# Kernel tuning notes

Hardware: AMD Instinct MI355X
Metric: run time of the kernel (lower is better)

The kernel has to match this reference:

```python
import jax, jax.numpy as jnp
import numpy as np

LOG2 = float(np.log(2.0))

def ssp(x):
    # shifted softplus: softplus(x) - log(2)
    return jax.nn.softplus(x) - LOG2

def setup_inputs() -> dict:
    key = jax.random.key(0)
    ks = jax.random.split(key, 16)
    N, E, F = 50000, 800000, 128  # atoms, interactions, feature/filter dim
    s = 0.05
    return {
        "x": jax.random.normal(ks[0], (N, F), jnp.float32),
        "dijk": jax.random.uniform(ks[1], (E, F), jnp.float32),
        "idx_j": jax.random.randint(ks[2], (E,), 0, N),
        "seg_i": jnp.sort(jax.random.randint(ks[3], (E,), 0, N)),
        "seg_j": jnp.arange(E),
        "seg_i_sum": N,
        "W1": jax.random.normal(ks[4], (F, F), jnp.float32) * s,
        "b1": jnp.zeros((F,), jnp.float32),
        "W2": jax.random.normal(ks[5], (F, F), jnp.float32) * s,
        "b2": jnp.zeros((F,), jnp.float32),
        "W_in2fac": jax.random.normal(ks[6], (F, F), jnp.float32) * s,
        "W_fac2out": jax.random.normal(ks[7], (F, F), jnp.float32) * s,
        "b_fac2out": jnp.zeros((F,), jnp.float32),
        "W_dense": jax.random.normal(ks[8], (F, F), jnp.float32) * s,
        "b_dense": jnp.zeros((F,), jnp.float32),
    }

def reference(x, dijk, idx_j, seg_i, seg_j, seg_i_sum,
              W1, b1, W2, b2, W_in2fac, W_fac2out, b_fac2out, W_dense, b_dense):
    E = dijk.shape[0]
    # --- CFnetFilter: dense -> dense -> segment-sum over seg_j ---
    h = ssp(dijk @ W1 + b1)                        # [E, F]
    w_ijk = ssp(h @ W2 + b2)                       # [E, F]
    w_ij = jax.ops.segment_sum(w_ijk, seg_j, num_segments=E)  # [E, F]
    # --- CFConv: in2fac -> gather idx_j -> filter mult -> segment-sum seg_i -> fac2out ---
    f = x @ W_in2fac                               # [N, F]
    f = f[idx_j]                                   # gather, [E, F]
    wf = w_ij * f                                  # [E, F]
    conv = jax.ops.segment_sum(wf, seg_i, num_segments=seg_i_sum)  # [N, F]
    c = ssp(conv @ W_fac2out + b_fac2out)          # [N, F]
    # --- residual dense ---
    v = c @ W_dense + b_dense                      # [N, F]
    y = x + v
    return (y, v)
```

## Files before the change

kernel.cpp:

```cpp
#include <hip/hip_runtime.h>

#define F 128

typedef __attribute__((ext_vector_type(8))) short bf16x8;
typedef __attribute__((ext_vector_type(4))) float f32x4;


__device__ __forceinline__ short f2bf(float f) {
  union { float f; unsigned u; } v; v.f = f;
  unsigned r = (v.u + 0x7FFFu + ((v.u >> 16) & 1u)) >> 16;
  return (short)r;
}

__device__ __forceinline__ unsigned cvt_pk_bf16(float a, float b) {
  unsigned d;
  asm("v_cvt_pk_bf16_f32 %0, %1, %2" : "=v"(d) : "v"(a), "v"(b));
  return d;
}

__device__ __forceinline__ float sspf(float x) {
  float t = __expf(-fabsf(x));
  return fmaxf(x, 0.0f) + __logf(1.0f + t) - 0.69314718055994530942f;
}

__device__ __forceinline__ int h_idx(int row, int k) {
  int chunk = k >> 3;
  int sw = chunk ^ (row & 15);
  return row * 128 + sw * 8 + (k & 7);
}

__device__ __forceinline__ int wfb_idx(int row, int c) {
  return row * 128 + (c ^ ((row & 4) << 2));
}

__device__ __forceinline__ bf16x8 load_bfrag_g(const unsigned short* __restrict__ W,
                                               int nt, int kb, int lane) {
  return *(const bf16x8*)(W + (((nt * 4 + kb) * 64 + lane) << 3));
}

__device__ __forceinline__ bf16x8 load_afrag_f32(const float* __restrict__ p, bool valid) {
  union { bf16x8 v; unsigned u[4]; } r;
  if (valid) {
    const float4* q = (const float4*)p;
    float4 x0 = q[0], x1 = q[1];
    r.u[0] = cvt_pk_bf16(x0.x, x0.y);
    r.u[1] = cvt_pk_bf16(x0.z, x0.w);
    r.u[2] = cvt_pk_bf16(x1.x, x1.y);
    r.u[3] = cvt_pk_bf16(x1.z, x1.w);
  } else {
    r.u[0] = r.u[1] = r.u[2] = r.u[3] = 0u;
  }
  return r.v;
}

__global__ void prep_weights(const float* __restrict__ W1, const float* __restrict__ W2,
                             const float* __restrict__ Wi2f, const float* __restrict__ Wf2o,
                             const float* __restrict__ Wd, unsigned short* __restrict__ out) {
  int t = blockIdx.x * 256 + threadIdx.x;
  int m = t >> 14;
  int idx = t & 16383;
  int k = idx >> 7, n = idx & 127;
  const float* W = (m == 0) ? W1 : (m == 1) ? W2 : (m == 2) ? Wi2f : (m == 3) ? Wf2o : Wd;
  float v = W[idx];
  int nt = n >> 4, kb = k >> 5;
  int lane = (((k >> 3) & 3) << 4) | (n & 15);
  int j = k & 7;
  int dst = (((nt * 4 + kb) * 64 + lane) << 3) | j;
  out[(m << 14) + dst] = (unsigned short)f2bf(v);
}

__global__ __launch_bounds__(256, 4) void f_kernel(const float* __restrict__ x,
                                                   const unsigned short* __restrict__ wfrag,
                                                   float* __restrict__ f, int N) {
  const int tid = threadIdx.x;
  const int lane = tid & 63, wv = tid >> 6;
  const int quad = lane >> 4, ln = lane & 15;
  const int r0 = blockIdx.x * 128;
  const unsigned short* Wf = wfrag + 2 * 16384;

  bf16x8 a1[2][4];
#pragma unroll
  for (int mt = 0; mt < 2; ++mt) {
    int row = r0 + wv * 32 + mt * 16 + ln;
    bool valid = row < N;
    const float* rp = x + (size_t)row * F + quad * 8;
#pragma unroll
    for (int kb = 0; kb < 4; ++kb) a1[mt][kb] = load_afrag_f32(rp + kb * 32, valid);
  }

#pragma unroll
  for (int nt = 0; nt < 8; ++nt) {
    f32x4 acc0 = {0, 0, 0, 0}, acc1 = {0, 0, 0, 0};
#pragma unroll
    for (int kb = 0; kb < 4; ++kb) {
      bf16x8 b = load_bfrag_g(Wf, nt, kb, lane);
      acc0 = __builtin_amdgcn_mfma_f32_16x16x32_bf16(a1[0][kb], b, acc0, 0, 0, 0);
      acc1 = __builtin_amdgcn_mfma_f32_16x16x32_bf16(a1[1][kb], b, acc1, 0, 0, 0);
    }
    int col = nt * 16 + ln;
#pragma unroll
    for (int mt = 0; mt < 2; ++mt) {
#pragma unroll
      for (int r = 0; r < 4; ++r) {
        int row = r0 + wv * 32 + mt * 16 + quad * 4 + r;
        if (row < N) f[(size_t)row * F + col] = (mt == 0) ? acc0[r] : acc1[r];
      }
    }
  }
}

__global__ __launch_bounds__(256, 4) void edge_kernel(
    const float* __restrict__ dijk, const int* __restrict__ idx_j, const int* __restrict__ seg_i,
    const float* __restrict__ b1, const float* __restrict__ b2,
    const unsigned short* __restrict__ wfrag, const float* __restrict__ f,
    float* __restrict__ conv, int E) {
  __shared__ union { short s[16384]; float fl[8192]; } sm;
  __shared__ int sIdx[128];
  __shared__ int sSeg[128];

  const int tid = threadIdx.x;
  const int lane = tid & 63, wv = tid >> 6;
  const int quad = lane >> 4, ln = lane & 15;
  const int e0 = blockIdx.x * 128;
  const unsigned short* W1f = wfrag;
  const unsigned short* W2f = wfrag + 16384;

  if (tid < 128) {
    int e = e0 + tid;
    sIdx[tid] = (e < E) ? idx_j[e] : 0;
    sSeg[tid] = (e < E) ? seg_i[e] : -1;
  }

  float bias1v[8], bias2v[8];
#pragma unroll
  for (int nt = 0; nt < 8; ++nt) {
    bias1v[nt] = b1[nt * 16 + ln];
    bias2v[nt] = b2[nt * 16 + ln];
  }

  bf16x8 a1[2][4];
#pragma unroll
  for (int mt = 0; mt < 2; ++mt) {
    int row = e0 + wv * 32 + mt * 16 + ln;
    bool valid = row < E;
    const float* rp = dijk + (size_t)row * F + quad * 8;
#pragma unroll
    for (int kb = 0; kb < 4; ++kb) a1[mt][kb] = load_afrag_f32(rp + kb * 32, valid);
  }

  short* sH = sm.s;
#pragma unroll
  for (int nt = 0; nt < 8; ++nt) {
    f32x4 acc0 = {0, 0, 0, 0}, acc1 = {0, 0, 0, 0};
#pragma unroll
    for (int kb = 0; kb < 4; ++kb) {
      bf16x8 b = load_bfrag_g(W1f, nt, kb, lane);
      acc0 = __builtin_amdgcn_mfma_f32_16x16x32_bf16(a1[0][kb], b, acc0, 0, 0, 0);
      acc1 = __builtin_amdgcn_mfma_f32_16x16x32_bf16(a1[1][kb], b, acc1, 0, 0, 0);
    }
    int c = nt * 16 + ln;
#pragma unroll
    for (int r = 0; r < 4; ++r) {
      sH[h_idx(wv * 32 + quad * 4 + r, c)] =
          (short)cvt_pk_bf16(sspf(acc0[r] + bias1v[nt]), 0.0f);
      sH[h_idx(wv * 32 + 16 + quad * 4 + r, c)] =
          (short)cvt_pk_bf16(sspf(acc1[r] + bias1v[nt]), 0.0f);
    }
  }
  __syncthreads();

  bf16x8 a2[2][4];
#pragma unroll
  for (int mt = 0; mt < 2; ++mt) {
    int row = wv * 32 + mt * 16 + ln;
#pragma unroll
    for (int kb = 0; kb < 4; ++kb)
      a2[mt][kb] = *(const bf16x8*)(sH + h_idx(row, kb * 32 + quad * 8));
  }

  float* sWF = sm.fl;
#pragma unroll
  for (int half = 0; half < 2; ++half) {
    float wreg[8][4];
#pragma unroll
    for (int nt = 0; nt < 8; ++nt) {
      f32x4 acc = {0, 0, 0, 0};
#pragma unroll
      for (int kb = 0; kb < 4; ++kb) {
        bf16x8 b = load_bfrag_g(W2f, nt, kb, lane);
        acc = __builtin_amdgcn_mfma_f32_16x16x32_bf16(a2[half][kb], b, acc, 0, 0, 0);
      }
#pragma unroll
      for (int r = 0; r < 4; ++r) wreg[nt][r] = sspf(acc[r] + bias2v[nt]);
    }

    __syncthreads();

#pragma unroll
    for (int r = 0; r < 4; ++r) {
      int lr = quad * 4 + r;
      int brow = wv * 16 + lr;
      int erow = wv * 32 + half * 16 + lr;
      int jrow = sIdx[erow];
      const float* fp = f + (size_t)jrow * F;
#pragma unroll
      for (int nt = 0; nt < 8; ++nt) {
        int c = nt * 16 + ln;
        sWF[wfb_idx(brow, c)] = wreg[nt][r] * fp[c];
      }
    }
    __syncthreads();

    {
      int c = tid & 127;
      int sub = tid >> 7;
      int b0 = sub * 32;
      float acc = 0.0f;
      int cur = sSeg[((b0 >> 4) << 5) + half * 16 + (b0 & 15)];
      for (int b = b0; b < b0 + 32; ++b) {
        int act = ((b >> 4) << 5) + half * 16 + (b & 15);
        int s = sSeg[act];
        if (s != cur) {
          if (cur >= 0) atomicAdd(conv + (size_t)cur * F + c, acc);
          acc = 0.0f; cur = s;
        }
        acc += sWF[wfb_idx(b, c)];
      }
      if (cur >= 0) atomicAdd(conv + (size_t)cur * F + c, acc);
    }
  }
}

__global__ __launch_bounds__(256, 4) void node_kernel(
    const float* __restrict__ conv, const float* __restrict__ x,
    const float* __restrict__ bf2o, const float* __restrict__ bd,
    const unsigned short* __restrict__ wfrag, float* __restrict__ y,
    float* __restrict__ vout, int N) {
  __shared__ short sC[16384];
  const int tid = threadIdx.x;
  const int lane = tid & 63, wv = tid >> 6;
  const int quad = lane >> 4, ln = lane & 15;
  const int r0 = blockIdx.x * 128;
  const unsigned short* Wa = wfrag + 3 * 16384;
  const unsigned short* Wd = wfrag + 4 * 16384;

  float bfv[8], bdv[8];
#pragma unroll
  for (int nt = 0; nt < 8; ++nt) {
    bfv[nt] = bf2o[nt * 16 + ln];
    bdv[nt] = bd[nt * 16 + ln];
  }

  bf16x8 a1[2][4];
#pragma unroll
  for (int mt = 0; mt < 2; ++mt) {
    int row = r0 + wv * 32 + mt * 16 + ln;
    bool valid = row < N;
    const float* rp = conv + (size_t)row * F + quad * 8;
#pragma unroll
    for (int kb = 0; kb < 4; ++kb) a1[mt][kb] = load_afrag_f32(rp + kb * 32, valid);
  }

#pragma unroll
  for (int nt = 0; nt < 8; ++nt) {
    f32x4 acc0 = {0, 0, 0, 0}, acc1 = {0, 0, 0, 0};
#pragma unroll
    for (int kb = 0; kb < 4; ++kb) {
      bf16x8 b = load_bfrag_g(Wa, nt, kb, lane);
      acc0 = __builtin_amdgcn_mfma_f32_16x16x32_bf16(a1[0][kb], b, acc0, 0, 0, 0);
      acc1 = __builtin_amdgcn_mfma_f32_16x16x32_bf16(a1[1][kb], b, acc1, 0, 0, 0);
    }
    int c = nt * 16 + ln;
#pragma unroll
    for (int r = 0; r < 4; ++r) {
      sC[h_idx(wv * 32 + quad * 4 + r, c)] =
          (short)cvt_pk_bf16(sspf(acc0[r] + bfv[nt]), 0.0f);
      sC[h_idx(wv * 32 + 16 + quad * 4 + r, c)] =
          (short)cvt_pk_bf16(sspf(acc1[r] + bfv[nt]), 0.0f);
    }
  }
  __syncthreads();

  bf16x8 a2[2][4];
#pragma unroll
  for (int mt = 0; mt < 2; ++mt) {
    int row = wv * 32 + mt * 16 + ln;
#pragma unroll
    for (int kb = 0; kb < 4; ++kb)
      a2[mt][kb] = *(const bf16x8*)(sC + h_idx(row, kb * 32 + quad * 8));
  }

#pragma unroll
  for (int nt = 0; nt < 8; ++nt) {
    f32x4 acc0 = {0, 0, 0, 0}, acc1 = {0, 0, 0, 0};
#pragma unroll
    for (int kb = 0; kb < 4; ++kb) {
      bf16x8 b = load_bfrag_g(Wd, nt, kb, lane);
      acc0 = __builtin_amdgcn_mfma_f32_16x16x32_bf16(a2[0][kb], b, acc0, 0, 0, 0);
      acc1 = __builtin_amdgcn_mfma_f32_16x16x32_bf16(a2[1][kb], b, acc1, 0, 0, 0);
    }
    int col = nt * 16 + ln;
#pragma unroll
    for (int mt = 0; mt < 2; ++mt) {
#pragma unroll
      for (int r = 0; r < 4; ++r) {
        int row = r0 + wv * 32 + mt * 16 + quad * 4 + r;
        if (row < N) {
          float v = ((mt == 0) ? acc0[r] : acc1[r]) + bdv[nt];
          size_t o = (size_t)row * F + col;
          y[o] = x[o] + v;
          vout[o] = v;
        }
      }
    }
  }
}

extern "C" void kernel_launch(void* const* d_in, const int* in_sizes, int n_in,
                              void* d_out, int out_size, void* d_ws, size_t ws_size,
                              hipStream_t stream) {
  const float* x    = (const float*)d_in[0];
  const float* dijk = (const float*)d_in[1];
  const int*   idxj = (const int*)d_in[2];
  const int*   segi = (const int*)d_in[3];
  const float* W1   = (const float*)d_in[6];
  const float* b1   = (const float*)d_in[7];
  const float* W2   = (const float*)d_in[8];
  const float* b2   = (const float*)d_in[9];
  const float* Wi2f = (const float*)d_in[10];
  const float* Wf2o = (const float*)d_in[11];
  const float* bf2o = (const float*)d_in[12];
  const float* Wd   = (const float*)d_in[13];
  const float* bd   = (const float*)d_in[14];

  int N = in_sizes[0] / F;
  int E = in_sizes[1] / F;

  unsigned short* wfrag = (unsigned short*)d_ws;
  float* fbuf = (float*)((char*)d_ws + 5 * 16384 * sizeof(unsigned short));
  float* conv = fbuf + (size_t)N * F;

  float* y = (float*)d_out;
  float* vout = y + (size_t)N * F;

  hipMemsetAsync(conv, 0, (size_t)N * F * sizeof(float), stream);
  prep_weights<<<320, 256, 0, stream>>>(W1, W2, Wi2f, Wf2o, Wd, wfrag);

  int nb = (N + 127) / 128;
  int eb = (E + 127) / 128;
  f_kernel<<<nb, 256, 0, stream>>>(x, wfrag, fbuf, N);
  edge_kernel<<<eb, 256, 0, stream>>>(dijk, idxj, segi, b1, b2, wfrag, fbuf, conv, E);
  node_kernel<<<nb, 256, 0, stream>>>(conv, x, bf2o, bd, wfrag, y, vout, N);
}
```

Measured before the change: 991.5 us.

## Fuse filter product into edge epilogue with register segmented atomics, shrink node tiles

The edge kernel now multiplies the second-layer filter output by the gathered f rows straight from the MFMA accumulators. It sums runs of equal seg_i across each lane's 4 consecutive rows and issues atomics directly, which removes the shared-memory staging buffer, the index/segment preload and several block barriers. The conv zeroing memset is folded into f_kernel as a grid-stride loop. f_kernel and node_kernel move to 64-row tiles with one M-tile per wave. sspf is rewritten as log2(1+exp(x)) scaled, and the E-bound checks are dropped. The trade-off is roughly one atomic per 4 edges per column instead of one per segment per 32-row block. The new softplus can overflow exp for large inputs, and the kernel now assumes E is a multiple of 128.

```diff
diff --git a/kernel.cpp b/kernel.cpp
--- a/kernel.cpp
+++ b/kernel.cpp
@@ -19,18 +19,15 @@
 }
 
 __device__ __forceinline__ float sspf(float x) {
-  float t = __expf(-fabsf(x));
-  return fmaxf(x, 0.0f) + __logf(1.0f + t) - 0.69314718055994530942f;
+  return fmaf(0.69314718055994530942f,
+              __log2f(1.0f + __expf(x)),
+              -0.69314718055994530942f);
 }
 
 __device__ __forceinline__ int h_idx(int row, int k) {
   int chunk = k >> 3;
   int sw = chunk ^ (row & 15);
   return row * 128 + sw * 8 + (k & 7);
-}
-
-__device__ __forceinline__ int wfb_idx(int row, int c) {
-  return row * 128 + (c ^ ((row & 4) << 2));
 }
 
 __device__ __forceinline__ bf16x8 load_bfrag_g(const unsigned short* __restrict__ W,
@@ -69,42 +66,44 @@
   out[(m << 14) + dst] = (unsigned short)f2bf(v);
 }
 
-__global__ __launch_bounds__(256, 4) void f_kernel(const float* __restrict__ x,
+__global__ __launch_bounds__(256, 2) void f_kernel(const float* __restrict__ x,
                                                    const unsigned short* __restrict__ wfrag,
-                                                   float* __restrict__ f, int N) {
+                                                   float* __restrict__ f,
+                                                   float* __restrict__ conv, int N) {
   const int tid = threadIdx.x;
   const int lane = tid & 63, wv = tid >> 6;
   const int quad = lane >> 4, ln = lane & 15;
-  const int r0 = blockIdx.x * 128;
+
+  {
+    float4 z = {0.f, 0.f, 0.f, 0.f};
+    size_t total4 = (size_t)N * F / 4;
+    for (size_t i = (size_t)blockIdx.x * 256 + tid; i < total4; i += (size_t)gridDim.x * 256)
+      ((float4*)conv)[i] = z;
+  }
+
+  const int r0 = blockIdx.x * 64;
   const unsigned short* Wf = wfrag + 2 * 16384;
 
-  bf16x8 a1[2][4];
-#pragma unroll
-  for (int mt = 0; mt < 2; ++mt) {
-    int row = r0 + wv * 32 + mt * 16 + ln;
-    bool valid = row < N;
-    const float* rp = x + (size_t)row * F + quad * 8;
-#pragma unroll
-    for (int kb = 0; kb < 4; ++kb) a1[mt][kb] = load_afrag_f32(rp + kb * 32, valid);
-  }
-
-#pragma unroll
-  for (int nt = 0; nt < 8; ++nt) {
-    f32x4 acc0 = {0, 0, 0, 0}, acc1 = {0, 0, 0, 0};
+  int arow = r0 + wv * 16 + ln;
+  bool valid = arow < N;
+  const float* rp = x + (size_t)arow * F + quad * 8;
+  bf16x8 a1[4];
+#pragma unroll
+  for (int kb = 0; kb < 4; ++kb) a1[kb] = load_afrag_f32(rp + kb * 32, valid);
+
+#pragma unroll
+  for (int nt = 0; nt < 8; ++nt) {
+    f32x4 acc = {0, 0, 0, 0};
 #pragma unroll
     for (int kb = 0; kb < 4; ++kb) {
       bf16x8 b = load_bfrag_g(Wf, nt, kb, lane);
-      acc0 = __builtin_amdgcn_mfma_f32_16x16x32_bf16(a1[0][kb], b, acc0, 0, 0, 0);
-      acc1 = __builtin_amdgcn_mfma_f32_16x16x32_bf16(a1[1][kb], b, acc1, 0, 0, 0);
+      acc = __builtin_amdgcn_mfma_f32_16x16x32_bf16(a1[kb], b, acc, 0, 0, 0);
     }
     int col = nt * 16 + ln;
 #pragma unroll
-    for (int mt = 0; mt < 2; ++mt) {
-#pragma unroll
-      for (int r = 0; r < 4; ++r) {
-        int row = r0 + wv * 32 + mt * 16 + quad * 4 + r;
-        if (row < N) f[(size_t)row * F + col] = (mt == 0) ? acc0[r] : acc1[r];
-      }
+    for (int r = 0; r < 4; ++r) {
+      int row = r0 + wv * 16 + quad * 4 + r;
+      if (row < N) f[(size_t)row * F + col] = acc[r];
     }
   }
 }
@@ -114,10 +113,7 @@
     const float* __restrict__ b1, const float* __restrict__ b2,
     const unsigned short* __restrict__ wfrag, const float* __restrict__ f,
     float* __restrict__ conv, int E) {
-  __shared__ union { short s[16384]; float fl[8192]; } sm;
-  __shared__ int sIdx[128];
-  __shared__ int sSeg[128];
-
+  __shared__ short sH[16384];
   const int tid = threadIdx.x;
   const int lane = tid & 63, wv = tid >> 6;
   const int quad = lane >> 4, ln = lane & 15;
@@ -125,30 +121,18 @@
   const unsigned short* W1f = wfrag;
   const unsigned short* W2f = wfrag + 16384;
 
-  if (tid < 128) {
-    int e = e0 + tid;
-    sIdx[tid] = (e < E) ? idx_j[e] : 0;
-    sSeg[tid] = (e < E) ? seg_i[e] : -1;
-  }
-
-  float bias1v[8], bias2v[8];
-#pragma unroll
-  for (int nt = 0; nt < 8; ++nt) {
-    bias1v[nt] = b1[nt * 16 + ln];
-    bias2v[nt] = b2[nt * 16 + ln];
-  }
+  float bias1v[8];
+#pragma unroll
+  for (int nt = 0; nt < 8; ++nt) bias1v[nt] = b1[nt * 16 + ln];
 
   bf16x8 a1[2][4];
 #pragma unroll
   for (int mt = 0; mt < 2; ++mt) {
-    int row = e0 + wv * 32 + mt * 16 + ln;
-    bool valid = row < E;
-    const float* rp = dijk + (size_t)row * F + quad * 8;
-#pragma unroll
-    for (int kb = 0; kb < 4; ++kb) a1[mt][kb] = load_afrag_f32(rp + kb * 32, valid);
-  }
-
-  short* sH = sm.s;
+    const float* rp = dijk + (size_t)(e0 + wv * 32 + mt * 16 + ln) * F + quad * 8;
+#pragma unroll
+    for (int kb = 0; kb < 4; ++kb) a1[mt][kb] = load_afrag_f32(rp + kb * 32, true);
+  }
+
 #pragma unroll
   for (int nt = 0; nt < 8; ++nt) {
     f32x4 acc0 = {0, 0, 0, 0}, acc1 = {0, 0, 0, 0};
@@ -167,80 +151,66 @@
           (short)cvt_pk_bf16(sspf(acc1[r] + bias1v[nt]), 0.0f);
     }
   }
-  __syncthreads();
-
-  bf16x8 a2[2][4];
+
+  float bias2v[8];
+#pragma unroll
+  for (int nt = 0; nt < 8; ++nt) bias2v[nt] = b2[nt * 16 + ln];
+
 #pragma unroll
   for (int mt = 0; mt < 2; ++mt) {
-    int row = wv * 32 + mt * 16 + ln;
+    bf16x8 a2[4];
 #pragma unroll
     for (int kb = 0; kb < 4; ++kb)
-      a2[mt][kb] = *(const bf16x8*)(sH + h_idx(row, kb * 32 + quad * 8));
-  }
-
-  float* sWF = sm.fl;
-#pragma unroll
-  for (int half = 0; half < 2; ++half) {
-    float wreg[8][4];
+      a2[kb] = *(const bf16x8*)(sH + h_idx(wv * 32 + mt * 16 + ln, kb * 32 + quad * 8));
+
+    int r4 = e0 + wv * 32 + mt * 16 + quad * 4;
+    int4 sg = *(const int4*)(seg_i + r4);
+    int4 jr = *(const int4*)(idx_j + r4);
+    const float* f0 = f + (size_t)jr.x * F;
+    const float* f1 = f + (size_t)jr.y * F;
+    const float* f2 = f + (size_t)jr.z * F;
+    const float* f3 = f + (size_t)jr.w * F;
+    float* c0 = conv + (size_t)sg.x * F;
+    float* c1 = conv + (size_t)sg.y * F;
+    float* c2 = conv + (size_t)sg.z * F;
+    float* c3 = conv + (size_t)sg.w * F;
+    bool cut1 = sg.y != sg.x, cut2 = sg.z != sg.y, cut3 = sg.w != sg.z;
+
 #pragma unroll
     for (int nt = 0; nt < 8; ++nt) {
       f32x4 acc = {0, 0, 0, 0};
 #pragma unroll
       for (int kb = 0; kb < 4; ++kb) {
         bf16x8 b = load_bfrag_g(W2f, nt, kb, lane);
-        acc = __builtin_amdgcn_mfma_f32_16x16x32_bf16(a2[half][kb], b, acc, 0, 0, 0);
+        acc = __builtin_amdgcn_mfma_f32_16x16x32_bf16(a2[kb], b, acc, 0, 0, 0);
       }
-#pragma unroll
-      for (int r = 0; r < 4; ++r) wreg[nt][r] = sspf(acc[r] + bias2v[nt]);
-    }
-
-    __syncthreads();
-
-#pragma unroll
-    for (int r = 0; r < 4; ++r) {
-      int lr = quad * 4 + r;
-      int brow = wv * 16 + lr;
-      int erow = wv * 32 + half * 16 + lr;
-      int jrow = sIdx[erow];
-      const float* fp = f + (size_t)jrow * F;
-#pragma unroll
-      for (int nt = 0; nt < 8; ++nt) {
-        int c = nt * 16 + ln;
-        sWF[wfb_idx(brow, c)] = wreg[nt][r] * fp[c];
-      }
-    }
-    __syncthreads();
-
-    {
-      int c = tid & 127;
-      int sub = tid >> 7;
-      int b0 = sub * 32;
-      float acc = 0.0f;
-      int cur = sSeg[((b0 >> 4) << 5) + half * 16 + (b0 & 15)];
-      for (int b = b0; b < b0 + 32; ++b) {
-        int act = ((b >> 4) << 5) + half * 16 + (b & 15);
-        int s = sSeg[act];
-        if (s != cur) {
-          if (cur >= 0) atomicAdd(conv + (size_t)cur * F + c, acc);
-          acc = 0.0f; cur = s;
-        }
-        acc += sWF[wfb_idx(b, c)];
-      }
-      if (cur >= 0) atomicAdd(conv + (size_t)cur * F + c, acc);
-    }
-  }
-}
-
-__global__ __launch_bounds__(256, 4) void node_kernel(
+      int c = nt * 16 + ln;
+      float w0 = sspf(acc[0] + bias2v[nt]) * f0[c];
+      float w1 = sspf(acc[1] + bias2v[nt]) * f1[c];
+      float w2 = sspf(acc[2] + bias2v[nt]) * f2[c];
+      float w3 = sspf(acc[3] + bias2v[nt]) * f3[c];
+      float a = w0;
+      if (cut1) { atomicAdd(c0 + c, a); a = 0.0f; }
+      a += w1;
+      if (cut2) { atomicAdd(c1 + c, a); a = 0.0f; }
+      a += w2;
+      if (cut3) { atomicAdd(c2 + c, a); a = 0.0f; }
+      a += w3;
+      atomicAdd(c3 + c, a);
+    }
+  }
+}
+
+__global__ __launch_bounds__(256, 2) void node_kernel(
     const float* __restrict__ conv, const float* __restrict__ x,
     const float* __restrict__ bf2o, const float* __restrict__ bd,
     const unsigned short* __restrict__ wfrag, float* __restrict__ y,
     float* __restrict__ vout, int N) {
-  __shared__ short sC[16384];
+  __shared__ short sC[8192];
   const int tid = threadIdx.x;
   const int lane = tid & 63, wv = tid >> 6;
   const int quad = lane >> 4, ln = lane & 15;
-  const int r0 = blockIdx.x * 128;
+  const int r0 = blockIdx.x * 64;
   const unsigned short* Wa = wfrag + 3 * 16384;
   const unsigned short* Wd = wfrag + 4 * 16384;
 
@@ -251,66 +221,50 @@
     bdv[nt] = bd[nt * 16 + ln];
   }
 
-  bf16x8 a1[2][4];
-#pragma unroll
-  for (int mt = 0; mt < 2; ++mt) {
-    int row = r0 + wv * 32 + mt * 16 + ln;
-    bool valid = row < N;
-    const float* rp = conv + (size_t)row * F + quad * 8;
-#pragma unroll
-    for (int kb = 0; kb < 4; ++kb) a1[mt][kb] = load_afrag_f32(rp + kb * 32, valid);
-  }
-
-#pragma unroll
-  for (int nt = 0; nt < 8; ++nt) {
-    f32x4 acc0 = {0, 0, 0, 0}, acc1 = {0, 0, 0, 0};
+  int arow = r0 + wv * 16 + ln;
+  bool valid = arow < N;
+  const float* rp = conv + (size_t)arow * F + quad * 8;
+  bf16x8 a1[4];
+#pragma unroll
+  for (int kb = 0; kb < 4; ++kb) a1[kb] = load_afrag_f32(rp + kb * 32, valid);
+
+#pragma unroll
+  for (int nt = 0; nt < 8; ++nt) {
+    f32x4 acc = {0, 0, 0, 0};
 #pragma unroll
     for (int kb = 0; kb < 4; ++kb) {
       bf16x8 b = load_bfrag_g(Wa, nt, kb, lane);
-      acc0 = __builtin_amdgcn_mfma_f32_16x16x32_bf16(a1[0][kb], b, acc0, 0, 0, 0);
-      acc1 = __builtin_amdgcn_mfma_f32_16x16x32_bf16(a1[1][kb], b, acc1, 0, 0, 0);
+      acc = __builtin_amdgcn_mfma_f32_16x16x32_bf16(a1[kb], b, acc, 0, 0, 0);
     }
     int c = nt * 16 + ln;
 #pragma unroll
-    for (int r = 0; r < 4; ++r) {
-      sC[h_idx(wv * 32 + quad * 4 + r, c)] =
-          (short)cvt_pk_bf16(sspf(acc0[r] + bfv[nt]), 0.0f);
-      sC[h_idx(wv * 32 + 16 + quad * 4 + r, c)] =
-          (short)cvt_pk_bf16(sspf(acc1[r] + bfv[nt]), 0.0f);
-    }
-  }
-  __syncthreads();
-
-  bf16x8 a2[2][4];
-#pragma unroll
-  for (int mt = 0; mt < 2; ++mt) {
-    int row = wv * 32 + mt * 16 + ln;
-#pragma unroll
-    for (int kb = 0; kb < 4; ++kb)
-      a2[mt][kb] = *(const bf16x8*)(sC + h_idx(row, kb * 32 + quad * 8));
-  }
-
-#pragma unroll
-  for (int nt = 0; nt < 8; ++nt) {
-    f32x4 acc0 = {0, 0, 0, 0}, acc1 = {0, 0, 0, 0};
+    for (int r = 0; r < 4; ++r)
+      sC[h_idx(wv * 16 + quad * 4 + r, c)] =
+          (short)cvt_pk_bf16(sspf(acc[r] + bfv[nt]), 0.0f);
+  }
+
+  bf16x8 a2[4];
+#pragma unroll
+  for (int kb = 0; kb < 4; ++kb)
+    a2[kb] = *(const bf16x8*)(sC + h_idx(wv * 16 + ln, kb * 32 + quad * 8));
+
+#pragma unroll
+  for (int nt = 0; nt < 8; ++nt) {
+    f32x4 acc = {0, 0, 0, 0};
 #pragma unroll
     for (int kb = 0; kb < 4; ++kb) {
       bf16x8 b = load_bfrag_g(Wd, nt, kb, lane);
-      acc0 = __builtin_amdgcn_mfma_f32_16x16x32_bf16(a2[0][kb], b, acc0, 0, 0, 0);
-      acc1 = __builtin_amdgcn_mfma_f32_16x16x32_bf16(a2[1][kb], b, acc1, 0, 0, 0);
+      acc = __builtin_amdgcn_mfma_f32_16x16x32_bf16(a2[kb], b, acc, 0, 0, 0);
     }
     int col = nt * 16 + ln;
 #pragma unroll
-    for (int mt = 0; mt < 2; ++mt) {
-#pragma unroll
-      for (int r = 0; r < 4; ++r) {
-        int row = r0 + wv * 32 + mt * 16 + quad * 4 + r;
-        if (row < N) {
-          float v = ((mt == 0) ? acc0[r] : acc1[r]) + bdv[nt];
-          size_t o = (size_t)row * F + col;
-          y[o] = x[o] + v;
-          vout[o] = v;
-        }
+    for (int r = 0; r < 4; ++r) {
+      int row = r0 + wv * 16 + quad * 4 + r;
+      if (row < N) {
+        float v = acc[r] + bdv[nt];
+        size_t o = (size_t)row * F + col;
+        y[o] = x[o] + v;
+        vout[o] = v;
       }
     }
   }
@@ -343,12 +297,11 @@
   float* y = (float*)d_out;
   float* vout = y + (size_t)N * F;
 
-  hipMemsetAsync(conv, 0, (size_t)N * F * sizeof(float), stream);
   prep_weights<<<320, 256, 0, stream>>>(W1, W2, Wi2f, Wf2o, Wd, wfrag);
 
-  int nb = (N + 127) / 128;
+  int nb = (N + 63) / 64;
   int eb = (E + 127) / 128;
-  f_kernel<<<nb, 256, 0, stream>>>(x, wfrag, fbuf, N);
+  f_kernel<<<nb, 256, 0, stream>>>(x, wfrag, fbuf, conv, N);
   edge_kernel<<<eb, 256, 0, stream>>>(dijk, idxj, segi, b1, b2, wfrag, fbuf, conv, E);
   node_kernel<<<nb, 256, 0, stream>>>(conv, x, bf2o, bd, wfrag, y, vout, N);
 }
```

Result: faster. 922.9 us (-6.9%).
